# Kernel optimization log

Measured on AMD Instinct MI355X. Metric: run time of the kernel, lower is better.

The kernel has to match this reference:

```python
import jax, jax.numpy as jnp
import numpy as np

N_NODES = 100000
N_EDGES = 3200000
D_FEAT = 128
HIDDEN = 16
N_CLASSES = 7


def gcn_conv(x, edge_index, edge_weight, W, b, n_nodes):
    h = x @ W  # dense projection first (Fout small)
    src, dst = edge_index[0], edge_index[1]
    # add self-loops with weight 1
    loop = jnp.arange(n_nodes, dtype=edge_index.dtype)
    src_a = jnp.concatenate([src, loop])
    dst_a = jnp.concatenate([dst, loop])
    ew_a = jnp.concatenate([edge_weight, jnp.ones((n_nodes,), dtype=x.dtype)])
    deg = jax.ops.segment_sum(ew_a, dst_a, num_segments=n_nodes)
    dinv = jnp.where(deg > 0, jax.lax.rsqrt(deg), 0.0)
    norm = dinv[src_a] * ew_a * dinv[dst_a]  # [E+N]
    msg = h[src_a] * norm[:, None]  # gather + scale
    out = jax.ops.segment_sum(msg, dst_a, num_segments=n_nodes)
    return out + b


def setup_inputs() -> dict:
    key = jax.random.key(0)
    k = jax.random.split(key, 8)
    x = jax.random.normal(k[0], (N_NODES, D_FEAT), dtype=jnp.float32)
    edge_index = jax.random.randint(k[1], (2, N_EDGES), 0, N_NODES, dtype=jnp.int64)
    edge_weight = jax.random.uniform(k[2], (N_EDGES,), dtype=jnp.float32)
    s1 = 1.0 / np.sqrt(D_FEAT)
    s2 = 1.0 / np.sqrt(HIDDEN)
    W1 = jax.random.uniform(k[3], (D_FEAT, HIDDEN), jnp.float32, -s1, s1)
    b1 = jnp.zeros((HIDDEN,), jnp.float32)
    W2 = jax.random.uniform(k[4], (HIDDEN, N_CLASSES), jnp.float32, -s2, s2)
    b2 = jnp.zeros((N_CLASSES,), jnp.float32)
    return {"x": x, "edge_index": edge_index, "edge_weight": edge_weight,
            "W1": W1, "b1": b1, "W2": W2, "b2": b2}


def reference(x, edge_index, edge_weight, W1, b1, W2, b2):
    h = jax.nn.relu(gcn_conv(x, edge_index, edge_weight, W1, b1, N_NODES))
    out = gcn_conv(h, edge_index, edge_weight, W2, b2, N_NODES)
    return jax.nn.log_softmax(out, axis=1)
```

## Files before the change

### kernel.cpp

```cpp
#include <hip/hip_runtime.h>
#include <hip/hip_fp16.h>
#include <math.h>

constexpr int NN = 100000;
constexpr int NE = 3200000;
constexpr int DF = 128;
constexpr int NH = 16;
constexpr int NC = 7;

constexpr int BN    = 128;
constexpr int NB    = (NN + BN - 1) / BN;
constexpr int CAP   = 4608;
constexpr int CHUNK = 8192;
constexpr int AB    = (NE + CHUNK - 1) / CHUNK;
constexpr int EPT   = CHUNK / 1024;
constexpr int SPT   = (CAP + 1023) / 1024;

constexpr float QS   = 32767.0f;
constexpr float QINV = 1.0f / 32767.0f;

typedef _Float16 half8 __attribute__((ext_vector_type(8)));
typedef float    f32x4 __attribute__((ext_vector_type(4)));

__global__ void k_zero(int* __restrict__ gcur) {
    int t = blockIdx.x * blockDim.x + threadIdx.x;
    if (t < NB) gcur[t] = 0;
}

__global__ void __launch_bounds__(1024)
k_append(const int* __restrict__ src,
         const int* __restrict__ dst,
         const float* __restrict__ w,
         int* __restrict__ gcur,
         uint2* __restrict__ ebuf) {
    __shared__ int hist[NB];
    __shared__ int basev[NB];
    for (int i = threadIdx.x; i < NB; i += 1024) hist[i] = 0;
    __syncthreads();
    int e0 = blockIdx.x * CHUNK;
    unsigned slo[EPT], sw[EPT];
    int sbr[EPT];
#pragma unroll
    for (int k = 0; k < EPT; ++k) {
        int e = e0 + (int)threadIdx.x + k * 1024;
        sbr[k] = -1;
        if (e < NE) {
            int d = __builtin_nontemporal_load(dst + e);
            int b = d >> 7;
            int r = atomicAdd(&hist[b], 1);
            slo[k] = ((unsigned)(d & (BN - 1)) << 17) |
                     (unsigned)__builtin_nontemporal_load(src + e);
            sw[k]  = __float_as_uint(__builtin_nontemporal_load(w + e));
            sbr[k] = (b << 14) | r;
        }
    }
    __syncthreads();
    for (int b = threadIdx.x; b < NB; b += 1024) {
        int c = hist[b];
        basev[b] = (c > 0) ? atomicAdd(&gcur[b], c) : 0;
    }
    __syncthreads();
#pragma unroll
    for (int k = 0; k < EPT; ++k) {
        if (sbr[k] >= 0) {
            int b = sbr[k] >> 14;
            int pos = basev[b] + (sbr[k] & 0x3FFF);
            if (pos < CAP) {
                uint2 v; v.x = slo[k]; v.y = sw[k];
                ebuf[(size_t)b * CAP + pos] = v;
            }
        }
    }
}

__global__ void __launch_bounds__(1024)
k_sort(const int* __restrict__ gcur,
       uint2* __restrict__ ebuf,
       int* __restrict__ rs,
       int* __restrict__ rc,
       float* __restrict__ dinv) {
    __shared__ int cursor[BN];
    __shared__ int scanS[BN];
    __shared__ int startEx[BN];
    __shared__ unsigned sorted[CAP];
    int b = blockIdx.x;
    int tid = threadIdx.x;
    int cnt = min(gcur[b], CAP);
    const uint2* eb = ebuf + (size_t)b * CAP;
    if (tid < BN) cursor[tid] = 0;
    __syncthreads();
    unsigned sval[SPT];
    int sdr[SPT];
#pragma unroll
    for (int k = 0; k < SPT; ++k) {
        int i = tid + k * 1024;
        sdr[k] = -1;
        if (i < cnt) {
            uint2 v = eb[i];
            int dl = (v.x >> 17) & (BN - 1);
            unsigned q = (unsigned)(__uint_as_float(v.y) * QS + 0.5f);
            int r = atomicAdd(&cursor[dl], 1);
            sval[k] = (v.x & 0x1FFFF) | (q << 17);
            sdr[k] = (dl << 13) | r;
        }
    }
    __syncthreads();
    if (tid < BN) scanS[tid] = cursor[tid];
    __syncthreads();
    for (int off = 1; off < BN; off <<= 1) {
        int v = (tid < BN && tid >= off) ? scanS[tid - off] : 0;
        __syncthreads();
        if (tid < BN) scanS[tid] += v;
        __syncthreads();
    }
    if (tid < BN) {
        int ex = scanS[tid] - cursor[tid];
        startEx[tid] = ex;
        int n = b * BN + tid;
        if (n < NN) { rs[n] = b * CAP * 2 + ex; rc[n] = cursor[tid]; }
    }
    __syncthreads();
#pragma unroll
    for (int k = 0; k < SPT; ++k) {
        if (sdr[k] >= 0)
            sorted[startEx[sdr[k] >> 13] + (sdr[k] & 0x1FFF)] = sval[k];
    }
    __syncthreads();
    unsigned* eb32 = (unsigned*)ebuf + (size_t)b * CAP * 2;
    for (int i = tid; i < cnt; i += 1024) eb32[i] = sorted[i];
    if (tid < BN) {
        int n = b * BN + tid;
        if (n < NN) {
            float s = 1.0f;
            int s0 = startEx[tid], c = cursor[tid];
            for (int i = 0; i < c; ++i) s += (float)(sorted[s0 + i] >> 17) * QINV;
            dinv[n] = rsqrtf(s);
        }
    }
}

__global__ void __launch_bounds__(256)
k_proj1(const float* __restrict__ x,
        const float* __restrict__ W1,
        const float* __restrict__ dinv,
        __half* __restrict__ h1p) {
    int wave = threadIdx.x >> 6;
    int lane = threadIdx.x & 63;
    int tile = blockIdx.x * 4 + wave;
    if (tile * 16 >= NN) return;
    int m    = lane & 15;
    int quad = lane >> 4;
    half8 bfrag[4];
#pragma unroll
    for (int kc = 0; kc < 4; ++kc)
#pragma unroll
        for (int j = 0; j < 8; ++j)
            bfrag[kc][j] = (_Float16)W1[(kc * 32 + quad * 8 + j) * NH + m];
    int base = tile * 16;
    const float* xr = x + (size_t)(base + m) * DF + quad * 8;
    f32x4 acc = {0.f, 0.f, 0.f, 0.f};
#pragma unroll
    for (int kc = 0; kc < 4; ++kc) {
        const float4* p = (const float4*)(xr + kc * 32);
        float4 u0 = p[0];
        float4 u1 = p[1];
        half8 afrag;
        afrag[0] = (_Float16)u0.x; afrag[1] = (_Float16)u0.y;
        afrag[2] = (_Float16)u0.z; afrag[3] = (_Float16)u0.w;
        afrag[4] = (_Float16)u1.x; afrag[5] = (_Float16)u1.y;
        afrag[6] = (_Float16)u1.z; afrag[7] = (_Float16)u1.w;
        acc = __builtin_amdgcn_mfma_f32_16x16x32_f16(afrag, bfrag[kc], acc, 0, 0, 0);
    }
    float4 d4 = *(const float4*)(dinv + base + quad * 4);
#pragma unroll
    for (int reg = 0; reg < 4; ++reg) {
        float dd = (reg == 0) ? d4.x : (reg == 1) ? d4.y : (reg == 2) ? d4.z : d4.w;
        int row = quad * 4 + reg;
        h1p[(size_t)(base + row) * 16 + m] = __float2half(acc[reg] * dd);
    }
}

__global__ void __launch_bounds__(1024)
k_agg1p(const int* __restrict__ rs,
        const int* __restrict__ rc,
        const unsigned* __restrict__ cbuf,
        const __half* __restrict__ h1p,
        const float* __restrict__ dinv,
        const float* __restrict__ b1,
        const float* __restrict__ W2,
        __half* __restrict__ h2p) {
    const __half2* hp = (const __half2*)h1p;
    int t = blockIdx.x * 1024 + threadIdx.x;
    int n = t >> 3;
    int f2 = t & 7;
    if (n >= NN) return;
    float2 g0 = __half22float2(hp[n * 8 + f2]);
    float ax = g0.x, ay = g0.y;
    int s0 = rs[n], c = rc[n];
    int i = 0;
    for (; i + 1 < c; i += 2) {
        unsigned e0 = cbuf[s0 + i];
        unsigned e1 = cbuf[s0 + i + 1];
        float2 v0 = __half22float2(hp[(e0 & 0x1FFFF) * 8 + f2]);
        float2 v1 = __half22float2(hp[(e1 & 0x1FFFF) * 8 + f2]);
        float w0 = (float)(e0 >> 17) * QINV;
        float w1 = (float)(e1 >> 17) * QINV;
        ax += w0 * v0.x + w1 * v1.x;
        ay += w0 * v0.y + w1 * v1.y;
    }
    if (i < c) {
        unsigned e0 = cbuf[s0 + i];
        float2 v0 = __half22float2(hp[(e0 & 0x1FFFF) * 8 + f2]);
        float w0 = (float)(e0 >> 17) * QINV;
        ax += w0 * v0.x;
        ay += w0 * v0.y;
    }
    float di = dinv[n];
    float hr0 = fmaxf(di * ax + b1[2 * f2], 0.0f);
    float hr1 = fmaxf(di * ay + b1[2 * f2 + 1], 0.0f);
    float p[NC];
#pragma unroll
    for (int cc = 0; cc < NC; ++cc)
        p[cc] = hr0 * W2[(2 * f2) * NC + cc] + hr1 * W2[(2 * f2 + 1) * NC + cc];
#pragma unroll
    for (int mask = 1; mask < 8; mask <<= 1) {
#pragma unroll
        for (int cc = 0; cc < NC; ++cc)
            p[cc] += __shfl_xor(p[cc], mask, 8);
    }
    float tv = 0.0f;
#pragma unroll
    for (int cc = 0; cc < NC; ++cc)
        if (f2 == cc) tv = p[cc];
    h2p[n * 8 + f2] = __float2half(di * tv);
}

__global__ void __launch_bounds__(1024)
k_agg2_lsm(const int* __restrict__ rs,
           const int* __restrict__ rc,
           const unsigned* __restrict__ cbuf,
           const __half* __restrict__ h2p,
           const float* __restrict__ dinv,
           const float* __restrict__ b2,
           float* __restrict__ out) {
    const __half2* hp = (const __half2*)h2p;
    int t = blockIdx.x * 1024 + threadIdx.x;
    int n = t >> 2;
    int c2 = t & 3;
    if (n >= NN) return;
    float2 g0 = __half22float2(hp[n * 4 + c2]);
    float ax = g0.x, ay = g0.y;
    int s0 = rs[n], c = rc[n];
    int i = 0;
    for (; i + 1 < c; i += 2) {
        unsigned e0 = cbuf[s0 + i];
        unsigned e1 = cbuf[s0 + i + 1];
        float2 v0 = __half22float2(hp[(e0 & 0x1FFFF) * 4 + c2]);
        float2 v1 = __half22float2(hp[(e1 & 0x1FFFF) * 4 + c2]);
        float w0 = (float)(e0 >> 17) * QINV;
        float w1 = (float)(e1 >> 17) * QINV;
        ax += w0 * v0.x + w1 * v1.x;
        ay += w0 * v0.y + w1 * v1.y;
    }
    if (i < c) {
        unsigned e0 = cbuf[s0 + i];
        float2 v0 = __half22float2(hp[(e0 & 0x1FFFF) * 4 + c2]);
        float w0 = (float)(e0 >> 17) * QINV;
        ax += w0 * v0.x;
        ay += w0 * v0.y;
    }
    float di = dinv[n];
    float va = di * ax + b2[2 * c2];
    float vb = (c2 < 3) ? (di * ay + b2[2 * c2 + 1]) : -1e30f;
    float m = fmaxf(va, vb);
#pragma unroll
    for (int mask = 1; mask < 4; mask <<= 1)
        m = fmaxf(m, __shfl_xor(m, mask, 4));
    float s = __expf(va - m) + ((c2 < 3) ? __expf(vb - m) : 0.0f);
#pragma unroll
    for (int mask = 1; mask < 4; mask <<= 1)
        s += __shfl_xor(s, mask, 4);
    float lse = m + __logf(s);
    out[n * NC + 2 * c2] = va - lse;
    if (c2 < 3) out[n * NC + 2 * c2 + 1] = vb - lse;
}

extern "C" void kernel_launch(void* const* d_in, const int* in_sizes, int n_in,
                              void* d_out, int out_size, void* d_ws, size_t ws_size,
                              hipStream_t stream) {
    const float* x  = (const float*)d_in[0];
    const int*   ei = (const int*)d_in[1];
    const float* ew = (const float*)d_in[2];
    const float* W1 = (const float*)d_in[3];
    const float* b1 = (const float*)d_in[4];
    const float* W2 = (const float*)d_in[5];
    const float* b2 = (const float*)d_in[6];
    float* out = (float*)d_out;

    const int* srcp = ei;
    const int* dstp = ei + NE;

    float*  ws   = (float*)d_ws;
    float*  dinv = ws;
    __half* h1p  = (__half*)(ws + 100352);
    __half* h2p  = (__half*)(ws + 900352);
    int*    gcur = (int*)(ws + 1300352);
    int*    rs   = (int*)(ws + 1301376);
    int*    rc   = (int*)(ws + 1401728);
    uint2*  ebuf = (uint2*)(ws + 1502080);
    const unsigned* cbuf = (const unsigned*)ebuf;

    auto cdiv = [](long long a, long long b) { return (int)((a + b - 1) / b); };

    k_zero<<<1, 1024, 0, stream>>>(gcur);
    k_append<<<AB, 1024, 0, stream>>>(srcp, dstp, ew, gcur, ebuf);
    k_sort<<<NB, 1024, 0, stream>>>(gcur, ebuf, rs, rc, dinv);
    k_proj1<<<cdiv(NN, 64), 256, 0, stream>>>(x, W1, dinv, h1p);
    k_agg1p<<<cdiv((long long)NN * 8, 1024), 1024, 0, stream>>>(rs, rc, cbuf, h1p, dinv, b1, W2, h2p);
    k_agg2_lsm<<<cdiv((long long)NN * 4, 1024), 1024, 0, stream>>>(rs, rc, cbuf, h2p, dinv, b2, out);
}
```

Measured before the change: 232.7 us.

## Stage per-chunk edges in LDS by bucket and double destination bucket size

The append kernel now does a block-wide prefix scan over its per-bucket histogram. It places each edge into a bucket-sorted LDS staging array, then writes to the global bucket buffers in index order, so consecutive threads write contiguous runs within a bucket instead of scattered slots. Buckets now cover 256 destination nodes with doubled capacity, and chunks shrink to 4096 edges; the sort kernel's bit packing is adjusted to match. This adds LDS use, extra barriers and a 512-wide scan in exchange for better-coalesced scatter writes and fewer buckets.

```diff
diff --git a/kernel.cpp b/kernel.cpp
--- a/kernel.cpp
+++ b/kernel.cpp
@@ -8,10 +8,10 @@
 constexpr int NH = 16;
 constexpr int NC = 7;
 
-constexpr int BN    = 128;
+constexpr int BN    = 256;
 constexpr int NB    = (NN + BN - 1) / BN;
-constexpr int CAP   = 4608;
-constexpr int CHUNK = 8192;
+constexpr int CAP   = 9216;
+constexpr int CHUNK = 4096;
 constexpr int AB    = (NE + CHUNK - 1) / CHUNK;
 constexpr int EPT   = CHUNK / 1024;
 constexpr int SPT   = (CAP + 1023) / 1024;
@@ -34,7 +34,10 @@
          int* __restrict__ gcur,
          uint2* __restrict__ ebuf) {
     __shared__ int hist[NB];
+    __shared__ int cscan[512];
     __shared__ int basev[NB];
+    __shared__ uint2 staged[CHUNK];
+    __shared__ unsigned short sbkt[CHUNK];
     for (int i = threadIdx.x; i < NB; i += 1024) hist[i] = 0;
     __syncthreads();
     int e0 = blockIdx.x * CHUNK;
@@ -46,30 +49,48 @@
         sbr[k] = -1;
         if (e < NE) {
             int d = __builtin_nontemporal_load(dst + e);
-            int b = d >> 7;
+            int b = d >> 8;
             int r = atomicAdd(&hist[b], 1);
             slo[k] = ((unsigned)(d & (BN - 1)) << 17) |
                      (unsigned)__builtin_nontemporal_load(src + e);
             sw[k]  = __float_as_uint(__builtin_nontemporal_load(w + e));
-            sbr[k] = (b << 14) | r;
-        }
-    }
-    __syncthreads();
-    for (int b = threadIdx.x; b < NB; b += 1024) {
-        int c = hist[b];
-        basev[b] = (c > 0) ? atomicAdd(&gcur[b], c) : 0;
+            sbr[k] = (b << 13) | r;
+        }
+    }
+    __syncthreads();
+    {
+        int v0 = (threadIdx.x < NB) ? hist[threadIdx.x] : 0;
+        if (threadIdx.x < 512) cscan[threadIdx.x] = v0;
+        __syncthreads();
+        for (int off = 1; off < 512; off <<= 1) {
+            int v = (threadIdx.x < 512 && threadIdx.x >= off) ? cscan[threadIdx.x - off] : 0;
+            __syncthreads();
+            if (threadIdx.x < 512) cscan[threadIdx.x] += v;
+            __syncthreads();
+        }
+    }
+    if (threadIdx.x < NB) {
+        int c = hist[threadIdx.x];
+        basev[threadIdx.x] = (c > 0) ? atomicAdd(&gcur[threadIdx.x], c) : 0;
     }
     __syncthreads();
 #pragma unroll
     for (int k = 0; k < EPT; ++k) {
         if (sbr[k] >= 0) {
-            int b = sbr[k] >> 14;
-            int pos = basev[b] + (sbr[k] & 0x3FFF);
-            if (pos < CAP) {
-                uint2 v; v.x = slo[k]; v.y = sw[k];
-                ebuf[(size_t)b * CAP + pos] = v;
-            }
-        }
+            int b = sbr[k] >> 13;
+            int idx = (cscan[b] - hist[b]) + (sbr[k] & 0x1FFF);
+            uint2 v; v.x = slo[k]; v.y = sw[k];
+            staged[idx] = v;
+            sbkt[idx] = (unsigned short)b;
+        }
+    }
+    __syncthreads();
+    int total = min(CHUNK, NE - e0);
+    for (int i = threadIdx.x; i < total; i += 1024) {
+        int b = sbkt[i];
+        int st = cscan[b] - hist[b];
+        int pos = basev[b] + (i - st);
+        if (pos < CAP) ebuf[(size_t)b * CAP + pos] = staged[i];
     }
 }
 
@@ -101,7 +122,7 @@
             unsigned q = (unsigned)(__uint_as_float(v.y) * QS + 0.5f);
             int r = atomicAdd(&cursor[dl], 1);
             sval[k] = (v.x & 0x1FFFF) | (q << 17);
-            sdr[k] = (dl << 13) | r;
+            sdr[k] = (dl << 14) | r;
         }
     }
     __syncthreads();
@@ -123,7 +144,7 @@
 #pragma unroll
     for (int k = 0; k < SPT; ++k) {
         if (sdr[k] >= 0)
-            sorted[startEx[sdr[k] >> 13] + (sdr[k] & 0x1FFF)] = sval[k];
+            sorted[startEx[sdr[k] >> 14] + (sdr[k] & 0x3FFF)] = sval[k];
     }
     __syncthreads();
     unsigned* eb32 = (unsigned*)ebuf + (size_t)b * CAP * 2;
```

After: 226.0 us. 2.9% less time.
